# Optimization experiments

Hardware: AMD Instinct MI355X
Metric: run time of the kernel (lower is better)

The kernel has to match this reference:

```python
import jax, jax.numpy as jnp
import numpy as np

I_DIM, K_DIM, V_DIM, O_DIM = 64, 64, 32, 64
P, NH, NK = 7, 2, 4
B, H, W = 8, 256, 256


def get_unfold_params_v2(width, kernel_size, num_kernels):
    # exact replica of the torch helper's search
    if width <= kernel_size:
        return width, 1, 1, 1
    if width <= kernel_size + num_kernels:
        return kernel_size, 1, 1, width - kernel_size + 1

    def _sd(nk):
        d = 1
        while True:
            k = (kernel_size - 1) * d + 1
            if (width - k) % (nk - 1) == 0:
                return (width - k) // (nk - 1), d
            d += 1
            if d >= kernel_size:
                return None, d

    while True:
        s, d = _sd(num_kernels)
        if s and s < (kernel_size - 1) * d + 1:
            return kernel_size, s, d, num_kernels
        num_kernels += 1


def conv1x1(x, Wt, b):
    # x: [B,C,H,W], Wt: [O,C]
    return jnp.einsum('oc,bchw->bohw', Wt, x) + b[None, :, None, None]


def to_patches(x, nh, idx, p):
    # x: [B,C,H,W] -> [B, nh, nph*npw, C//nh, p*p] (unfold + rearrange)
    Bs, C, _, _ = x.shape
    hd = C // nh
    npw = idx.shape[0]
    pt = x[:, :, idx][:, :, :, :, idx]          # [B,C,nph,ph,npw,pw]
    pt = pt.reshape(Bs, nh, hd, npw, p, npw, p)
    pt = pt.transpose(0, 1, 3, 5, 2, 4, 6)       # B,nh,nph,npw,hd,ph,pw
    return pt.reshape(Bs, nh, npw * npw, hd, p * p)


def from_patches(o, nh, idx, p, Hh, Ww):
    # o: [B,nh,S,hd,p*p] -> fold (overlap scatter-add) -> [B, nh*hd, H, W]
    Bs, _, _, hd, _ = o.shape
    npw = idx.shape[0]
    o = o.reshape(Bs, nh, npw, npw, hd, p, p)
    o = o.transpose(0, 1, 4, 2, 5, 3, 6)         # B,nh,hd,nph,ph,npw,pw
    o = o.reshape(Bs, nh * hd, npw, p, npw, p)
    out = jnp.zeros((Bs, nh * hd, Hh, Ww), o.dtype)
    return out.at[:, :, idx[:, :, None, None], idx[None, None, :, :]].add(o)


def setup_inputs() -> dict:
    key = jax.random.key(0)
    ks = jax.random.split(key, 8)
    s = 0.05
    return {
        'x1': jax.random.normal(ks[0], (B, I_DIM, H, W), jnp.float32),
        'x2': jax.random.normal(ks[1], (B, I_DIM, H, W), jnp.float32),
        'Wk': jax.random.normal(ks[2], (2 * K_DIM, I_DIM), jnp.float32) * s,
        'bk': jax.random.normal(ks[3], (2 * K_DIM,), jnp.float32) * s,
        'Wv': jax.random.normal(ks[4], (2 * V_DIM, I_DIM), jnp.float32) * s,
        'bv': jax.random.normal(ks[5], (2 * V_DIM,), jnp.float32) * s,
        'Wp': jax.random.normal(ks[6], (O_DIM, 2 * V_DIM), jnp.float32) * s,
        'bp': jax.random.normal(ks[7], (O_DIM,), jnp.float32) * s,
    }


def reference(x1, x2, Wk, bk, Wv, bv, Wp, bp):
    _, _, Hh, Ww = x1.shape
    p, stride, dilation, nkrn = get_unfold_params_v2(Ww, P, NK)
    idx = np.arange(nkrn)[:, None] * stride + np.arange(p)[None, :] * dilation  # [npw,p]

    # grouped 1x1 convs (groups=2): split weights into per-stream halves
    k1 = conv1x1(x1, Wk[:K_DIM], bk[:K_DIM])
    k2 = conv1x1(x2, Wk[K_DIM:], bk[K_DIM:])
    v1 = conv1x1(x1, Wv[:V_DIM], bv[:V_DIM])
    v2 = conv1x1(x2, Wv[V_DIM:], bv[V_DIM:])

    k1p = to_patches(k1, NH, idx, p)  # [B,nh,S,hd_k,pp]
    k2p = to_patches(k2, NH, idx, p)
    v1p = to_patches(v1, NH, idx, p)  # [B,nh,S,hd_v,pp]
    v2p = to_patches(v2, NH, idx, p)

    scale = k1p.shape[-2] ** (-0.5)
    kk = jnp.einsum('bnsdx,bnsdy->bnsxy', k1p * scale, k2p)  # [B,nh,S,pp,pp]
    a1 = jax.nn.softmax(kk, axis=-2)
    o1 = jnp.einsum('bnsxy,bnsdx->bnsdy', a1, v1p)
    a2 = jax.nn.softmax(kk, axis=-1)
    o2 = jnp.einsum('bnsxy,bnsdy->bnsdx', a2, v2p)

    o1 = from_patches(o1, NH, idx, p, Hh, Ww)  # [B,V_DIM,H,W]
    o2 = from_patches(o2, NH, idx, p, Hh, Ww)
    o = jnp.concatenate([o1, o2], axis=1)      # [B,2*V_DIM,H,W]
    return conv1x1(o, Wp, bp)                  # [B,O_DIM,H,W]
```

## Files before the change

### kernel.cpp

```cpp
#include <hip/hip_runtime.h>

#define BB 8
#define HH 256
#define CIN 64
#define NPW 12
#define SPP 144
#define PP 49
#define PDIM 7
#define STRIDE 21
#define DIL 4
#define NS 84
#define HDK 32
#define HDV 16
#define RS 52

static __device__ __forceinline__ unsigned short f2bf(float f) {
  union { float f; unsigned u; } v; v.f = f;
  unsigned r = (v.u + 0x7fffu + ((v.u >> 16) & 1u)) >> 16;
  return (unsigned short)r;
}
static __device__ __forceinline__ float bf2f(unsigned short h) {
  union { unsigned u; float f; } v; v.u = ((unsigned)h) << 16;
  return v.f;
}

__global__ __launch_bounds__(256, 4) void k1_fused(
    const float* __restrict__ x1, const float* __restrict__ x2,
    const float* __restrict__ Wk, const float* __restrict__ bk,
    const float* __restrict__ Wv, const float* __restrict__ bv,
    const float* __restrict__ Wp, float* __restrict__ P)
{
  __shared__ unsigned short kv[192][RS];
  __shared__ union UU {
    unsigned short xs[2][CIN][RS];
    struct {
      unsigned short kkb[2][49][RS];
      unsigned short O[64][RS];
      float cmax[2][49], csum[2][49];
      float rmax[2][49], rsum[2][49];
    } a;
  } u;

  const int tid = threadIdx.x;
  const int blk = blockIdx.x;
  const int b  = blk / SPP;
  const int s  = blk % SPP;
  const int pi = s / NPW, pj = s % NPW;
  const int h0 = pi * STRIDE, w0 = pj * STRIDE;

  for (int i = tid; i < 2 * CIN * PP; i += 256) {
    int src = i / (CIN * PP);
    int r = i - src * (CIN * PP);
    int c = r / PP, t = r - c * PP;
    int ph = t / PDIM, pw = t - ph * PDIM;
    const float* xp = src ? x2 : x1;
    float v = xp[(((size_t)b * CIN + c) * HH + (h0 + ph * DIL)) * HH + (w0 + pw * DIL)];
    u.xs[src][c][t] = f2bf(v);
  }
  __syncthreads();

  for (int task = tid; task < 48 * 13; task += 256) {
    int g = task / 13, tg = task % 13;
    int row0 = g * 4, t0 = tg * 4;
    int src = (row0 < 64) ? 0 : (row0 < 128 ? 1 : (row0 < 160 ? 0 : 1));
    const float* wbase;
    float bias[4];
    if (row0 < 128) {
      wbase = Wk + row0 * 64;
      #pragma unroll
      for (int i = 0; i < 4; i++) bias[i] = bk[row0 + i];
    } else {
      wbase = Wv + (row0 - 128) * 64;
      #pragma unroll
      for (int i = 0; i < 4; i++) bias[i] = bv[row0 - 128 + i];
    }
    const unsigned short* xsrc = &u.xs[src][0][0];
    float acc[4][4];
    #pragma unroll
    for (int i = 0; i < 4; i++)
      #pragma unroll
      for (int j = 0; j < 4; j++) acc[i][j] = 0.f;
    for (int c = 0; c < 64; c++) {
      float wv0 = wbase[c], wv1 = wbase[64 + c], wv2 = wbase[128 + c], wv3 = wbase[192 + c];
      ushort4 x4 = *(const ushort4*)&xsrc[c * RS + t0];
      float xv[4] = { bf2f(x4.x), bf2f(x4.y), bf2f(x4.z), bf2f(x4.w) };
      #pragma unroll
      for (int j = 0; j < 4; j++) {
        acc[0][j] += wv0 * xv[j]; acc[1][j] += wv1 * xv[j];
        acc[2][j] += wv2 * xv[j]; acc[3][j] += wv3 * xv[j];
      }
    }
    #pragma unroll
    for (int i = 0; i < 4; i++)
      #pragma unroll
      for (int j = 0; j < 4; j++)
        if (t0 + j < PP) kv[row0 + i][t0 + j] = f2bf(acc[i][j] + bias[i]);
  }
  __syncthreads();

  const float scale = 0.17677669529663687f;

  if (tid < 182) {
    int n = tid / 91;
    int r = tid % 91;
    int xg = r / 7, yg = r % 7;
    int x0 = xg * 4, y0 = yg * 7;
    float acc[4][7];
    #pragma unroll
    for (int i = 0; i < 4; i++)
      #pragma unroll
      for (int j = 0; j < 7; j++) acc[i][j] = 0.f;
    for (int d = 0; d < HDK; d++) {
      const unsigned short* k1r = kv[n * HDK + d];
      const unsigned short* k2r = kv[64 + n * HDK + d];
      ushort4 a4 = *(const ushort4*)&k1r[x0];
      float av[4] = { bf2f(a4.x), bf2f(a4.y), bf2f(a4.z), bf2f(a4.w) };
      float bvv[7];
      #pragma unroll
      for (int j = 0; j < 7; j++) bvv[j] = bf2f(k2r[y0 + j]);
      #pragma unroll
      for (int i = 0; i < 4; i++)
        #pragma unroll
        for (int j = 0; j < 7; j++) acc[i][j] += av[i] * bvv[j];
    }
    #pragma unroll
    for (int i = 0; i < 4; i++)
      if (x0 + i < 49)
        #pragma unroll
        for (int j = 0; j < 7; j++)
          u.a.kkb[n][x0 + i][y0 + j] = f2bf(acc[i][j] * scale);
  }
  __syncthreads();

  if (tid < 196) {
    int n = tid / 98;
    int r = tid % 98;
    int isRow = r >= 49;
    int j = r - (isRow ? 49 : 0);
    float m = -1e30f;
    for (int k = 0; k < 49; k++) {
      float v = bf2f(isRow ? u.a.kkb[n][j][k] : u.a.kkb[n][k][j]);
      m = fmaxf(m, v);
    }
    float sm = 0.f;
    for (int k = 0; k < 49; k++) {
      float v = bf2f(isRow ? u.a.kkb[n][j][k] : u.a.kkb[n][k][j]);
      sm += __expf(v - m);
    }
    if (isRow) { u.a.rmax[n][j] = m; u.a.rsum[n][j] = 1.0f / sm; }
    else       { u.a.cmax[n][j] = m; u.a.csum[n][j] = 1.0f / sm; }
  }
  __syncthreads();

  if (tid < 208) {
    int n = tid / 104;
    int r = tid % 104;
    int side = r / 52;
    int r2 = r % 52;
    int dg = r2 / 13, tg = r2 % 13;
    int d0 = dg * 4, t0 = tg * 4;
    int tc[4];
    #pragma unroll
    for (int j = 0; j < 4; j++) tc[j] = min(t0 + j, 48);
    float acc[4][4];
    #pragma unroll
    for (int i = 0; i < 4; i++)
      #pragma unroll
      for (int j = 0; j < 4; j++) acc[i][j] = 0.f;
    if (side == 0) {
      float cm[4];
      #pragma unroll
      for (int j = 0; j < 4; j++) cm[j] = u.a.cmax[n][tc[j]];
      for (int x = 0; x < 49; x++) {
        ushort4 k4 = *(const ushort4*)&u.a.kkb[n][x][t0];
        float e[4] = { __expf(bf2f(k4.x) - cm[0]), __expf(bf2f(k4.y) - cm[1]),
                       __expf(bf2f(k4.z) - cm[2]), __expf(bf2f(k4.w) - cm[3]) };
        #pragma unroll
        for (int i = 0; i < 4; i++) {
          float vv = bf2f(kv[128 + n * HDV + d0 + i][x]);
          acc[i][0] += vv * e[0]; acc[i][1] += vv * e[1];
          acc[i][2] += vv * e[2]; acc[i][3] += vv * e[3];
        }
      }
      #pragma unroll
      for (int i = 0; i < 4; i++)
        #pragma unroll
        for (int j = 0; j < 4; j++)
          if (t0 + j < 49)
            u.a.O[n * HDV + d0 + i][t0 + j] = f2bf(acc[i][j] * u.a.csum[n][t0 + j]);
    } else {
      float rm[4];
      #pragma unroll
      for (int j = 0; j < 4; j++) rm[j] = u.a.rmax[n][tc[j]];
      for (int y = 0; y < 49; y++) {
        float e[4];
        #pragma unroll
        for (int j = 0; j < 4; j++)
          e[j] = __expf(bf2f(u.a.kkb[n][tc[j]][y]) - rm[j]);
        #pragma unroll
        for (int i = 0; i < 4; i++) {
          float vv = bf2f(kv[160 + n * HDV + d0 + i][y]);
          acc[i][0] += vv * e[0]; acc[i][1] += vv * e[1];
          acc[i][2] += vv * e[2]; acc[i][3] += vv * e[3];
        }
      }
      #pragma unroll
      for (int i = 0; i < 4; i++)
        #pragma unroll
        for (int j = 0; j < 4; j++)
          if (t0 + j < 49)
            u.a.O[32 + n * HDV + d0 + i][t0 + j] = f2bf(acc[i][j] * u.a.rsum[n][t0 + j]);
    }
  }
  __syncthreads();

  if (tid < 208) {
    int ocg = tid / 13, tg = tid % 13;
    int oc0 = ocg * 4, t0 = tg * 4;
    float acc[4][4];
    #pragma unroll
    for (int i = 0; i < 4; i++)
      #pragma unroll
      for (int j = 0; j < 4; j++) acc[i][j] = 0.f;
    #pragma unroll 4
    for (int l = 0; l < 64; l++) {
      float w0 = Wp[(oc0 + 0) * 64 + l];
      float w1 = Wp[(oc0 + 1) * 64 + l];
      float w2 = Wp[(oc0 + 2) * 64 + l];
      float w3 = Wp[(oc0 + 3) * 64 + l];
      ushort4 o4 = *(const ushort4*)&u.a.O[l][t0];
      float ov[4] = { bf2f(o4.x), bf2f(o4.y), bf2f(o4.z), bf2f(o4.w) };
      #pragma unroll
      for (int j = 0; j < 4; j++) {
        acc[0][j] += w0 * ov[j]; acc[1][j] += w1 * ov[j];
        acc[2][j] += w2 * ov[j]; acc[3][j] += w3 * ov[j];
      }
    }
    #pragma unroll
    for (int i = 0; i < 4; i++) {
      #pragma unroll
      for (int j = 0; j < 4; j++) {
        int t = t0 + j;
        if (t < 49) {
          int ph = t / 7, pw = t - ph * 7;
          P[(((size_t)b * 64 + (oc0 + i)) * NS + (pi * 7 + ph)) * NS + (pj * 7 + pw)] =
              acc[i][j];
        }
      }
    }
  }
}

__global__ __launch_bounds__(256) void k2_merge(
    const float* __restrict__ P, const float* __restrict__ bp,
    float* __restrict__ out)
{
  __shared__ float bps[64];
  __shared__ int wsmap[256];
  const int tid = threadIdx.x;
  const int b = blockIdx.x / HH, h = blockIdx.x % HH;
  if (tid < 64) bps[tid] = bp[tid];
  {
    int w = tid, wsv = -1;
    for (int pj = 0; pj < NPW; pj++) {
      int r = w - pj * STRIDE;
      if (r >= 0 && r <= (PDIM - 1) * DIL && (r % DIL) == 0) { wsv = pj * PDIM + r / DIL; break; }
    }
    wsmap[tid] = wsv;
  }
  int hs = -1;
  for (int pi = 0; pi < NPW; pi++) {
    int r = h - pi * STRIDE;
    if (r >= 0 && r <= (PDIM - 1) * DIL && (r % DIL) == 0) { hs = pi * PDIM + r / DIL; break; }
  }
  __syncthreads();

  const int wq = tid & 63;
  const int ocq = tid >> 6;
  float4* out4 = (float4*)out;

  if (hs < 0) {
    #pragma unroll 4
    for (int oc = ocq; oc < 64; oc += 4) {
      float bv = bps[oc];
      out4[(((size_t)b * 64 + oc) * HH + h) * 64 + wq] = make_float4(bv, bv, bv, bv);
    }
    return;
  }
  const int ws0 = wsmap[wq * 4 + 0], ws1 = wsmap[wq * 4 + 1];
  const int ws2 = wsmap[wq * 4 + 2], ws3 = wsmap[wq * 4 + 3];
  #pragma unroll 4
  for (int oc = ocq; oc < 64; oc += 4) {
    float bv = bps[oc];
    size_t rbase = (((size_t)b * 64 + oc) * NS + hs) * NS;
    float4 v = make_float4(bv, bv, bv, bv);
    if (ws0 >= 0) v.x += P[rbase + ws0];
    if (ws1 >= 0) v.y += P[rbase + ws1];
    if (ws2 >= 0) v.z += P[rbase + ws2];
    if (ws3 >= 0) v.w += P[rbase + ws3];
    out4[(((size_t)b * 64 + oc) * HH + h) * 64 + wq] = v;
  }
}

extern "C" void kernel_launch(void* const* d_in, const int* in_sizes, int n_in,
                              void* d_out, int out_size, void* d_ws, size_t ws_size,
                              hipStream_t stream) {
  const float* x1 = (const float*)d_in[0];
  const float* x2 = (const float*)d_in[1];
  const float* Wk = (const float*)d_in[2];
  const float* bk = (const float*)d_in[3];
  const float* Wv = (const float*)d_in[4];
  const float* bv = (const float*)d_in[5];
  const float* Wp = (const float*)d_in[6];
  const float* bp = (const float*)d_in[7];
  float* P = (float*)d_ws;
  float* out = (float*)d_out;

  k1_fused<<<dim3(BB * SPP), dim3(256), 0, stream>>>(x1, x2, Wk, bk, Wv, bv, Wp, P);
  k2_merge<<<dim3(BB * HH), dim3(256), 0, stream>>>(P, bp, out);
}
```

Baseline: 406.1 us.

## Move all fused-kernel matmul stages onto bf16 MFMA with swizzled LDS layouts

Every stage of the fused per-patch kernel now runs on 16x16x32 bf16 MFMA instructions instead of scalar FMA loops: the key/value projections, the key-key score matrix, both softmax-weighted value products and the output projection. Weights for the 1x1 convs are split into hi/lo bf16 pairs to recover near-fp32 accuracy, and the 49 patch positions are padded to 64. Shared memory is re-laid out with XOR swizzles so MFMA fragment loads avoid bank conflicts. In exchange, the padding adds wasted work, the extra split-weight MFMAs cost instructions, and occupancy is lowered to three blocks per CU.

```diff
diff --git a/kernel.cpp b/kernel.cpp
--- a/kernel.cpp
+++ b/kernel.cpp
@@ -10,9 +10,11 @@
 #define STRIDE 21
 #define DIL 4
 #define NS 84
-#define HDK 32
-#define HDV 16
-#define RS 52
+
+typedef __attribute__((ext_vector_type(8))) short bf16x8;
+typedef __attribute__((ext_vector_type(4))) float f32x4;
+
+#define MFMA(a, b, c) __builtin_amdgcn_mfma_f32_16x16x32_bf16((a), (b), (c), 0, 0, 0)
 
 static __device__ __forceinline__ unsigned short f2bf(float f) {
   union { float f; unsigned u; } v; v.f = f;
@@ -23,29 +25,30 @@
   union { unsigned u; float f; } v; v.u = ((unsigned)h) << 16;
   return v.f;
 }
-
-__global__ __launch_bounds__(256, 4) void k1_fused(
+static __device__ __forceinline__ unsigned pk2(float a, float b) {
+  return (unsigned)f2bf(a) | ((unsigned)f2bf(b) << 16);
+}
+
+__global__ __launch_bounds__(256, 3) void k1_fused(
     const float* __restrict__ x1, const float* __restrict__ x2,
     const float* __restrict__ Wk, const float* __restrict__ bk,
     const float* __restrict__ Wv, const float* __restrict__ bv,
     const float* __restrict__ Wp, float* __restrict__ P)
 {
-  __shared__ unsigned short kv[192][RS];
-  __shared__ union UU {
-    unsigned short xs[2][CIN][RS];
-    struct {
-      unsigned short kkb[2][49][RS];
-      unsigned short O[64][RS];
-      float cmax[2][49], csum[2][49];
-      float rmax[2][49], rsum[2][49];
-    } a;
-  } u;
+  __shared__ __align__(16) short uA[9216];
+  __shared__ __align__(16) short uB[8704];
+  __shared__ __align__(16) short sV[4096];
+  __shared__ float sStat[4][2][64];
 
   const int tid = threadIdx.x;
+  const int lane = tid & 63;
+  const int wid = tid >> 6;
+  const int l16 = lane & 15;
+  const int l4 = lane >> 4;
   const int blk = blockIdx.x;
   const int b  = blk / SPP;
-  const int s  = blk % SPP;
-  const int pi = s / NPW, pj = s % NPW;
+  const int sp = blk % SPP;
+  const int pi = sp / NPW, pj = sp % NPW;
   const int h0 = pi * STRIDE, w0 = pj * STRIDE;
 
   for (int i = tid; i < 2 * CIN * PP; i += 256) {
@@ -55,80 +58,95 @@
     int ph = t / PDIM, pw = t - ph * PDIM;
     const float* xp = src ? x2 : x1;
     float v = xp[(((size_t)b * CIN + c) * HH + (h0 + ph * DIL)) * HH + (w0 + pw * DIL)];
-    u.xs[src][c][t] = f2bf(v);
-  }
-  __syncthreads();
-
-  for (int task = tid; task < 48 * 13; task += 256) {
-    int g = task / 13, tg = task % 13;
-    int row0 = g * 4, t0 = tg * 4;
-    int src = (row0 < 64) ? 0 : (row0 < 128 ? 1 : (row0 < 160 ? 0 : 1));
-    const float* wbase;
-    float bias[4];
-    if (row0 < 128) {
-      wbase = Wk + row0 * 64;
-      #pragma unroll
-      for (int i = 0; i < 4; i++) bias[i] = bk[row0 + i];
-    } else {
-      wbase = Wv + (row0 - 128) * 64;
-      #pragma unroll
-      for (int i = 0; i < 4; i++) bias[i] = bv[row0 - 128 + i];
-    }
-    const unsigned short* xsrc = &u.xs[src][0][0];
-    float acc[4][4];
-    #pragma unroll
-    for (int i = 0; i < 4; i++)
-      #pragma unroll
-      for (int j = 0; j < 4; j++) acc[i][j] = 0.f;
-    for (int c = 0; c < 64; c++) {
-      float wv0 = wbase[c], wv1 = wbase[64 + c], wv2 = wbase[128 + c], wv3 = wbase[192 + c];
-      ushort4 x4 = *(const ushort4*)&xsrc[c * RS + t0];
-      float xv[4] = { bf2f(x4.x), bf2f(x4.y), bf2f(x4.z), bf2f(x4.w) };
-      #pragma unroll
-      for (int j = 0; j < 4; j++) {
-        acc[0][j] += wv0 * xv[j]; acc[1][j] += wv1 * xv[j];
-        acc[2][j] += wv2 * xv[j]; acc[3][j] += wv3 * xv[j];
-      }
-    }
-    #pragma unroll
-    for (int i = 0; i < 4; i++)
-      #pragma unroll
-      for (int j = 0; j < 4; j++)
-        if (t0 + j < PP) kv[row0 + i][t0 + j] = f2bf(acc[i][j] + bias[i]);
+    uA[(src * 64 + t) * 64 + ((((c >> 3) ^ (t & 7)) << 3) | (c & 7))] = (short)f2bf(v);
+  }
+  for (int i = tid; i < 2 * 15 * 64; i += 256) {
+    int src = i / (15 * 64);
+    int r = i - src * 15 * 64;
+    int t = 49 + (r >> 6);
+    int c = r & 63;
+    uA[(src * 64 + t) * 64 + c] = 0;
+  }
+  __syncthreads();
+
+  {
+    #pragma unroll
+    for (int mi = 0; mi < 3; mi++) {
+      const int m = wid * 3 + mi;
+      const int r0 = m * 16;
+      const int src = (m < 4) ? 0 : (m < 8 ? 1 : (m < 10 ? 0 : 1));
+      const int rl = r0 + l16;
+      const float* wrow = (r0 < 128) ? (Wk + (size_t)rl * 64)
+                                     : (Wv + (size_t)(rl - 128) * 64);
+      bf16x8 ahi[2], alo[2];
+      #pragma unroll
+      for (int kt = 0; kt < 2; kt++) {
+        const float* wp8 = wrow + kt * 32 + l4 * 8;
+        float4 wa = *(const float4*)wp8;
+        float4 wb = *(const float4*)(wp8 + 4);
+        float wf[8] = {wa.x, wa.y, wa.z, wa.w, wb.x, wb.y, wb.z, wb.w};
+        #pragma unroll
+        for (int j = 0; j < 8; j++) {
+          unsigned short h = f2bf(wf[j]);
+          ahi[kt][j] = (short)h;
+          alo[kt][j] = (short)f2bf(wf[j] - bf2f(h));
+        }
+      }
+      float bias[4];
+      #pragma unroll
+      for (int i = 0; i < 4; i++) {
+        int rd = r0 + l4 * 4 + i;
+        bias[i] = (r0 < 128) ? bk[rd] : bv[rd - 128];
+      }
+      #pragma unroll
+      for (int nt = 0; nt < 4; nt++) {
+        const int t = nt * 16 + l16;
+        f32x4 acc = {0.f, 0.f, 0.f, 0.f};
+        #pragma unroll
+        for (int kt = 0; kt < 2; kt++) {
+          bf16x8 xb = *(const bf16x8*)
+              &uA[(src * 64 + t) * 64 + ((((kt << 2) + l4) ^ (t & 7)) << 3)];
+          acc = MFMA(alo[kt], xb, acc);
+          acc = MFMA(ahi[kt], xb, acc);
+        }
+        if (r0 < 128) {
+          unsigned* p = (unsigned*)&uB[t * 136 + r0 + l4 * 4];
+          p[0] = pk2(acc[0] + bias[0], acc[1] + bias[1]);
+          p[1] = pk2(acc[2] + bias[2], acc[3] + bias[3]);
+        } else {
+          #pragma unroll
+          for (int i = 0; i < 4; i++) {
+            int rv = r0 - 128 + l4 * 4 + i;
+            sV[rv * 64 + ((((t >> 3) ^ (rv & 7)) << 3) | (t & 7))] =
+                (short)f2bf(acc[i] + bias[i]);
+          }
+        }
+      }
+    }
   }
   __syncthreads();
 
   const float scale = 0.17677669529663687f;
 
-  if (tid < 182) {
-    int n = tid / 91;
-    int r = tid % 91;
-    int xg = r / 7, yg = r % 7;
-    int x0 = xg * 4, y0 = yg * 7;
-    float acc[4][7];
-    #pragma unroll
-    for (int i = 0; i < 4; i++)
-      #pragma unroll
-      for (int j = 0; j < 7; j++) acc[i][j] = 0.f;
-    for (int d = 0; d < HDK; d++) {
-      const unsigned short* k1r = kv[n * HDK + d];
-      const unsigned short* k2r = kv[64 + n * HDK + d];
-      ushort4 a4 = *(const ushort4*)&k1r[x0];
-      float av[4] = { bf2f(a4.x), bf2f(a4.y), bf2f(a4.z), bf2f(a4.w) };
-      float bvv[7];
-      #pragma unroll
-      for (int j = 0; j < 7; j++) bvv[j] = bf2f(k2r[y0 + j]);
-      #pragma unroll
-      for (int i = 0; i < 4; i++)
-        #pragma unroll
-        for (int j = 0; j < 7; j++) acc[i][j] += av[i] * bvv[j];
-    }
-    #pragma unroll
-    for (int i = 0; i < 4; i++)
-      if (x0 + i < 49)
-        #pragma unroll
-        for (int j = 0; j < 7; j++)
-          u.a.kkb[n][x0 + i][y0 + j] = f2bf(acc[i][j] * scale);
+  {
+    const int n = wid >> 1;
+    #pragma unroll
+    for (int xi = 0; xi < 2; xi++) {
+      const int x0 = ((wid & 1) * 2 + xi) * 16;
+      bf16x8 a = *(const bf16x8*)&uB[(x0 + l16) * 136 + n * 32 + l4 * 8];
+      #pragma unroll
+      for (int yt = 0; yt < 4; yt++) {
+        const int y = yt * 16 + l16;
+        bf16x8 bb = *(const bf16x8*)&uB[y * 136 + 64 + n * 32 + l4 * 8];
+        f32x4 acc = {0.f, 0.f, 0.f, 0.f};
+        acc = MFMA(a, bb, acc);
+        #pragma unroll
+        for (int i = 0; i < 4; i++) {
+          int x = x0 + l4 * 4 + i;
+          uA[(n * 64 + x) * 72 + y] = (short)f2bf(acc[i] * scale);
+        }
+      }
+    }
   }
   __syncthreads();
 
@@ -137,114 +155,112 @@
     int r = tid % 98;
     int isRow = r >= 49;
     int j = r - (isRow ? 49 : 0);
-    float m = -1e30f;
+    float mx = -1e30f;
     for (int k = 0; k < 49; k++) {
-      float v = bf2f(isRow ? u.a.kkb[n][j][k] : u.a.kkb[n][k][j]);
-      m = fmaxf(m, v);
+      float v = bf2f((unsigned short)uA[(n * 64 + (isRow ? j : k)) * 72 + (isRow ? k : j)]);
+      mx = fmaxf(mx, v);
     }
     float sm = 0.f;
     for (int k = 0; k < 49; k++) {
-      float v = bf2f(isRow ? u.a.kkb[n][j][k] : u.a.kkb[n][k][j]);
-      sm += __expf(v - m);
-    }
-    if (isRow) { u.a.rmax[n][j] = m; u.a.rsum[n][j] = 1.0f / sm; }
-    else       { u.a.cmax[n][j] = m; u.a.csum[n][j] = 1.0f / sm; }
-  }
-  __syncthreads();
-
-  if (tid < 208) {
-    int n = tid / 104;
-    int r = tid % 104;
-    int side = r / 52;
-    int r2 = r % 52;
-    int dg = r2 / 13, tg = r2 % 13;
-    int d0 = dg * 4, t0 = tg * 4;
-    int tc[4];
-    #pragma unroll
-    for (int j = 0; j < 4; j++) tc[j] = min(t0 + j, 48);
-    float acc[4][4];
-    #pragma unroll
-    for (int i = 0; i < 4; i++)
-      #pragma unroll
-      for (int j = 0; j < 4; j++) acc[i][j] = 0.f;
+      float v = bf2f((unsigned short)uA[(n * 64 + (isRow ? j : k)) * 72 + (isRow ? k : j)]);
+      sm += __expf(v - mx);
+    }
+    int kind = isRow ? 2 : 0;
+    sStat[kind][n][j] = mx;
+    sStat[kind + 1][n][j] = 1.0f / sm;
+  }
+  __syncthreads();
+
+  {
+    const int n = wid >> 1;
+    const int side = wid & 1;
+    const int rv = side * 32 + n * 16 + l16;
+    bf16x8 av[2];
+    #pragma unroll
+    for (int kt = 0; kt < 2; kt++)
+      av[kt] = *(const bf16x8*)&sV[rv * 64 + ((((kt << 2) + l4) ^ (rv & 7)) << 3)];
     if (side == 0) {
-      float cm[4];
-      #pragma unroll
-      for (int j = 0; j < 4; j++) cm[j] = u.a.cmax[n][tc[j]];
-      for (int x = 0; x < 49; x++) {
-        ushort4 k4 = *(const ushort4*)&u.a.kkb[n][x][t0];
-        float e[4] = { __expf(bf2f(k4.x) - cm[0]), __expf(bf2f(k4.y) - cm[1]),
-                       __expf(bf2f(k4.z) - cm[2]), __expf(bf2f(k4.w) - cm[3]) };
+      #pragma unroll
+      for (int tt = 0; tt < 4; tt++) {
+        const int t = tt * 16 + l16;
+        const float cm = sStat[0][n][t], cs = sStat[1][n][t];
+        f32x4 acc = {0.f, 0.f, 0.f, 0.f};
+        #pragma unroll
+        for (int kt = 0; kt < 2; kt++) {
+          bf16x8 bfrag;
+          #pragma unroll
+          for (int j = 0; j < 8; j++) {
+            const int x = kt * 32 + l4 * 8 + j;
+            float v = bf2f((unsigned short)uA[(n * 64 + x) * 72 + t]);
+            float e = (x < PP) ? __expf(v - cm) : 0.f;
+            bfrag[j] = (short)f2bf(e);
+          }
+          acc = MFMA(av[kt], bfrag, acc);
+        }
+        unsigned* p = (unsigned*)&uB[t * 72 + n * 16 + l4 * 4];
+        p[0] = pk2(acc[0] * cs, acc[1] * cs);
+        p[1] = pk2(acc[2] * cs, acc[3] * cs);
+      }
+    } else {
+      #pragma unroll
+      for (int xt = 0; xt < 4; xt++) {
+        const int x = xt * 16 + l16;
+        const float rm = sStat[2][n][x], rs = sStat[3][n][x];
+        f32x4 acc = {0.f, 0.f, 0.f, 0.f};
+        #pragma unroll
+        for (int kt = 0; kt < 2; kt++) {
+          bf16x8 braw = *(const bf16x8*)&uA[(n * 64 + x) * 72 + kt * 32 + l4 * 8];
+          bf16x8 bfrag;
+          #pragma unroll
+          for (int j = 0; j < 8; j++) {
+            const int y = kt * 32 + l4 * 8 + j;
+            float v = bf2f((unsigned short)braw[j]);
+            float e = (y < PP) ? __expf(v - rm) : 0.f;
+            bfrag[j] = (short)f2bf(e);
+          }
+          acc = MFMA(av[kt], bfrag, acc);
+        }
+        unsigned* p = (unsigned*)&uB[x * 72 + 32 + n * 16 + l4 * 4];
+        p[0] = pk2(acc[0] * rs, acc[1] * rs);
+        p[1] = pk2(acc[2] * rs, acc[3] * rs);
+      }
+    }
+  }
+  __syncthreads();
+
+  {
+    const float* wrow = Wp + (size_t)(wid * 16 + l16) * 64;
+    bf16x8 whi[2], wlo[2];
+    #pragma unroll
+    for (int kt = 0; kt < 2; kt++) {
+      const float* wp8 = wrow + kt * 32 + l4 * 8;
+      float4 wa = *(const float4*)wp8;
+      float4 wb = *(const float4*)(wp8 + 4);
+      float wf[8] = {wa.x, wa.y, wa.z, wa.w, wb.x, wb.y, wb.z, wb.w};
+      #pragma unroll
+      for (int j = 0; j < 8; j++) {
+        unsigned short h = f2bf(wf[j]);
+        whi[kt][j] = (short)h;
+        wlo[kt][j] = (short)f2bf(wf[j] - bf2f(h));
+      }
+    }
+    #pragma unroll
+    for (int tt = 0; tt < 4; tt++) {
+      const int t = tt * 16 + l16;
+      f32x4 acc = {0.f, 0.f, 0.f, 0.f};
+      #pragma unroll
+      for (int kt = 0; kt < 2; kt++) {
+        bf16x8 ob = *(const bf16x8*)&uB[t * 72 + kt * 32 + l4 * 8];
+        acc = MFMA(wlo[kt], ob, acc);
+        acc = MFMA(whi[kt], ob, acc);
+      }
+      if (t < PP) {
+        const int ph = t / 7, pw = t - ph * 7;
+        const size_t col = (size_t)(pi * 7 + ph) * NS + (pj * 7 + pw);
         #pragma unroll
         for (int i = 0; i < 4; i++) {
-          float vv = bf2f(kv[128 + n * HDV + d0 + i][x]);
-          acc[i][0] += vv * e[0]; acc[i][1] += vv * e[1];
-          acc[i][2] += vv * e[2]; acc[i][3] += vv * e[3];
-        }
-      }
-      #pragma unroll
-      for (int i = 0; i < 4; i++)
-        #pragma unroll
-        for (int j = 0; j < 4; j++)
-          if (t0 + j < 49)
-            u.a.O[n * HDV + d0 + i][t0 + j] = f2bf(acc[i][j] * u.a.csum[n][t0 + j]);
-    } else {
-      float rm[4];
-      #pragma unroll
-      for (int j = 0; j < 4; j++) rm[j] = u.a.rmax[n][tc[j]];
-      for (int y = 0; y < 49; y++) {
-        float e[4];
-        #pragma unroll
-        for (int j = 0; j < 4; j++)
-          e[j] = __expf(bf2f(u.a.kkb[n][tc[j]][y]) - rm[j]);
-        #pragma unroll
-        for (int i = 0; i < 4; i++) {
-          float vv = bf2f(kv[160 + n * HDV + d0 + i][y]);
-          acc[i][0] += vv * e[0]; acc[i][1] += vv * e[1];
-          acc[i][2] += vv * e[2]; acc[i][3] += vv * e[3];
-        }
-      }
-      #pragma unroll
-      for (int i = 0; i < 4; i++)
-        #pragma unroll
-        for (int j = 0; j < 4; j++)
-          if (t0 + j < 49)
-            u.a.O[32 + n * HDV + d0 + i][t0 + j] = f2bf(acc[i][j] * u.a.rsum[n][t0 + j]);
-    }
-  }
-  __syncthreads();
-
-  if (tid < 208) {
-    int ocg = tid / 13, tg = tid % 13;
-    int oc0 = ocg * 4, t0 = tg * 4;
-    float acc[4][4];
-    #pragma unroll
-    for (int i = 0; i < 4; i++)
-      #pragma unroll
-      for (int j = 0; j < 4; j++) acc[i][j] = 0.f;
-    #pragma unroll 4
-    for (int l = 0; l < 64; l++) {
-      float w0 = Wp[(oc0 + 0) * 64 + l];
-      float w1 = Wp[(oc0 + 1) * 64 + l];
-      float w2 = Wp[(oc0 + 2) * 64 + l];
-      float w3 = Wp[(oc0 + 3) * 64 + l];
-      ushort4 o4 = *(const ushort4*)&u.a.O[l][t0];
-      float ov[4] = { bf2f(o4.x), bf2f(o4.y), bf2f(o4.z), bf2f(o4.w) };
-      #pragma unroll
-      for (int j = 0; j < 4; j++) {
-        acc[0][j] += w0 * ov[j]; acc[1][j] += w1 * ov[j];
-        acc[2][j] += w2 * ov[j]; acc[3][j] += w3 * ov[j];
-      }
-    }
-    #pragma unroll
-    for (int i = 0; i < 4; i++) {
-      #pragma unroll
-      for (int j = 0; j < 4; j++) {
-        int t = t0 + j;
-        if (t < 49) {
-          int ph = t / 7, pw = t - ph * 7;
-          P[(((size_t)b * 64 + (oc0 + i)) * NS + (pi * 7 + ph)) * NS + (pj * 7 + pw)] =
-              acc[i][j];
+          const int oc = wid * 16 + l4 * 4 + i;
+          P[((size_t)b * 64 + oc) * (NS * NS) + col] = acc[i];
         }
       }
     }
```

After: 332.9 us. -18.0%, faster.
